# Kernel optimization log

Hardware: AMD Instinct MI355X
Metric: run time of the kernel (lower is better)

## Reference

```python
import jax, jax.numpy as jnp
import numpy as np

K_NN = 5
COS_EPS = 1e-8  # torch cosine_similarity eps


def setup_inputs() -> dict:
    key = jax.random.key(0)
    ks = jax.random.split(key, 10)
    N1, N2, D, E, H = 2000, 2000, 63, 64, 8
    return {
        "lm_X": jax.random.normal(ks[0], (N1, D), jnp.float32),
        "lm_Y": jax.random.normal(ks[1], (N1, 2), jnp.float32),
        "tg_X": jax.random.normal(ks[2], (N2, D), jnp.float32),
        "tg_Y": jax.random.normal(ks[3], (N2, 2), jnp.float32),
        "lm_delay": jax.random.uniform(ks[4], (N1,), jnp.float32),
        "tg_delay": jax.random.uniform(ks[5], (N2,), jnp.float32),
        # learned params: embedding Linear(input_dim=D+1 -> E) and per-head score weights
        "W_emb": jax.random.normal(ks[6], (E, D + 1), jnp.float32) / np.sqrt(D + 1),
        "b_emb": jnp.zeros((E,), jnp.float32),
        "w1": jax.random.normal(ks[7], (E, H), jnp.float32),
        "w2": jax.random.normal(ks[8], (E, H), jnp.float32),
    }


def _knn_adj(X, k):
    # binary row-wise k-nearest-neighbour adjacency, self excluded
    n = X.shape[0]
    sq = jnp.sum(X * X, axis=1)
    d2 = sq[:, None] + sq[None, :] - 2.0 * (X @ X.T)  # [n, n] squared distances
    d2 = jnp.where(jnp.eye(n, dtype=bool), jnp.inf, d2)  # exclude self
    _, idx = jax.lax.top_k(-d2, k)  # k smallest distances -> [n, k]
    rows = jnp.arange(n)[:, None]
    return jnp.zeros((n, n), X.dtype).at[rows, idx].set(1.0)


def reference(lm_X, lm_Y, tg_X, tg_Y, lm_delay, tg_delay, W_emb, b_emb, w1, w2):
    N1 = lm_X.shape[0]
    N2 = tg_X.shape[0]
    N = N1 + N2
    k = K_NN

    # ---- community-KNN adjacency over landmarks, label aggregation ----
    adj_lm = _knn_adj(lm_X, k)                      # [N1, N1] binary, k ones per row
    y_pred = (adj_lm @ lm_Y) * (1.0 / k)            # [N1, 2]

    # ---- teacher adjacency: (1 - I) with lm block = adj_lm, tg block = 0 ----
    adj_teacher = 1.0 - jnp.eye(N, dtype=lm_X.dtype)
    adj_teacher = adj_teacher.at[:N1, :N1].set(adj_lm)
    adj_teacher = adj_teacher.at[N1:, N1:].set(0.0)

    # ---- node features + embedding ----
    lm_feat = jnp.concatenate([lm_X, lm_delay[:, None]], axis=1)  # [N1, D+1]
    tg_feat = jnp.concatenate([tg_X, tg_delay[:, None]], axis=1)  # [N2, D+1]
    feats = jnp.concatenate([lm_feat, tg_feat], axis=0)           # [N, D+1]
    e = feats @ W_emb.T + b_emb                                    # [N, E]

    # ---- multi-head cosine-similarity edge probabilities (all heads at once) ----
    a = e[:, None, :] * w1.T[None, :, :]            # [N, H, E] : e * w1[:, h]
    b = e[:, None, :] * w2.T[None, :, :]            # [N, H, E] : e * w2[:, h]
    na = jnp.linalg.norm(a, axis=-1)                # [N, H]
    nb = jnp.linalg.norm(b, axis=-1)                # [N, H]
    dot = jnp.einsum("nhe,mhe->nmh", a, b)          # [N, N, H]
    sim = dot / jnp.maximum(na[:, None, :] * nb[None, :, :], COS_EPS)
    alpha = jax.nn.sigmoid(sim)                      # [N, N, H]
    adj = jnp.mean(alpha, axis=-1)                   # [N, N]

    return (y_pred, adj, adj_teacher)
```

## Files before the change

kernel.cpp:

```cpp
#include <hip/hip_runtime.h>
#include <math.h>

#define N1 2000
#define N2 2000
#define NT 4000
#define D  63
#define E  64
#define H  8
#define KNN 5
#define NPAD 4032
#define MPAD 4096

typedef short bf16x8 __attribute__((ext_vector_type(8)));
typedef float f32x4  __attribute__((ext_vector_type(4)));

__device__ __forceinline__ unsigned short f2bf(float x) {
    unsigned u = __float_as_uint(x);
    u = (u + 0x7fffu + ((u >> 16) & 1u)) >> 16;
    return (unsigned short)u;
}

__global__ void k_sq(const float* __restrict__ X, float* __restrict__ sq) {
    int i = blockIdx.x * blockDim.x + threadIdx.x;
    if (i < N1) {
        float s = 0.f;
        for (int d = 0; d < D; ++d) { float v = X[i * D + d]; s += v * v; }
        sq[i] = s;
    }
}

__global__ __launch_bounds__(256) void k_d2(const float* __restrict__ X,
                                            const float* __restrict__ sq,
                                            float* __restrict__ d2) {
    __shared__ float Xi[64][68];
    __shared__ float Xj[64][68];
    int i0 = blockIdx.y * 64, j0 = blockIdx.x * 64;
    int tid = threadIdx.x;
    for (int t = tid; t < 64 * 64; t += 256) {
        int r = t >> 6, c = t & 63;
        int gi = min(i0 + r, N1 - 1);
        int gj = min(j0 + r, N1 - 1);
        Xi[r][c] = (c < D) ? X[gi * D + c] : 0.f;
        Xj[r][c] = (c < D) ? X[gj * D + c] : 0.f;
    }
    __syncthreads();
    int tx = tid & 15, ty = tid >> 4;
    float acc[4][4];
    #pragma unroll
    for (int a = 0; a < 4; ++a)
        #pragma unroll
        for (int b = 0; b < 4; ++b) acc[a][b] = 0.f;

    #pragma unroll 4
    for (int kk = 0; kk < 16; ++kk) {
        float4 av[4], bv[4];
        #pragma unroll
        for (int ii = 0; ii < 4; ++ii) av[ii] = *(const float4*)&Xi[ty + 16 * ii][4 * kk];
        #pragma unroll
        for (int jj = 0; jj < 4; ++jj) bv[jj] = *(const float4*)&Xj[tx + 16 * jj][4 * kk];
        #pragma unroll
        for (int ii = 0; ii < 4; ++ii)
            #pragma unroll
            for (int jj = 0; jj < 4; ++jj)
                acc[ii][jj] += av[ii].x * bv[jj].x + av[ii].y * bv[jj].y +
                               av[ii].z * bv[jj].z + av[ii].w * bv[jj].w;
    }

    #pragma unroll
    for (int ii = 0; ii < 4; ++ii) {
        int i = i0 + ty + 16 * ii;
        #pragma unroll
        for (int jj = 0; jj < 4; ++jj) {
            int j = j0 + tx + 16 * jj;
            if (i < N1 && j < N1) {
                float v = sq[i] + sq[j] - 2.f * acc[ii][jj];
                if (i == j) v = __builtin_inff();
                d2[i * N1 + j] = v;
            }
        }
    }
}

__device__ __forceinline__ bool dless(float d1, int i1, float d2v, int i2) {
    return d1 < d2v || (d1 == d2v && i1 < i2);
}

__device__ __forceinline__ void ins5(float bd[KNN], int bi[KNN], float d, int j) {
    if (dless(d, j, bd[KNN - 1], bi[KNN - 1])) {
        bd[KNN - 1] = d; bi[KNN - 1] = j;
        #pragma unroll
        for (int s = KNN - 1; s > 0; --s) {
            if (dless(bd[s], bi[s], bd[s - 1], bi[s - 1])) {
                float td = bd[s]; bd[s] = bd[s - 1]; bd[s - 1] = td;
                int ti = bi[s]; bi[s] = bi[s - 1]; bi[s - 1] = ti;
            }
        }
    }
}

__global__ __launch_bounds__(256) void k_top5(const float* __restrict__ d2,
                                              const float* __restrict__ lmY,
                                              float* __restrict__ ypred,
                                              int* __restrict__ idx) {
    __shared__ float sd[4 * KNN];
    __shared__ int   si[4 * KNN];
    int i = blockIdx.x;
    int tid = threadIdx.x;
    const float* row = d2 + i * N1;

    float bd[KNN]; int bi[KNN];
    #pragma unroll
    for (int s = 0; s < KNN; ++s) { bd[s] = __builtin_inff(); bi[s] = 0x7fffffff; }
    #pragma unroll
    for (int k = 0; k < 8; ++k) {
        int j = tid + k * 256;
        if (j < N1) ins5(bd, bi, row[j], j);
    }

    int lane = tid & 63, wave = tid >> 6;
    float wd[KNN]; int wi[KNN];
    #pragma unroll
    for (int s = 0; s < KNN; ++s) {
        float d = bd[0]; int ix = bi[0];
        #pragma unroll
        for (int m = 1; m < 64; m <<= 1) {
            float od = __shfl_xor(d, m, 64);
            int   oi = __shfl_xor(ix, m, 64);
            if (dless(od, oi, d, ix)) { d = od; ix = oi; }
        }
        wd[s] = d; wi[s] = ix;
        if (d == bd[0] && ix == bi[0]) {
            #pragma unroll
            for (int q = 0; q < KNN - 1; ++q) { bd[q] = bd[q + 1]; bi[q] = bi[q + 1]; }
            bd[KNN - 1] = __builtin_inff(); bi[KNN - 1] = 0x7fffffff;
        }
    }
    if (lane == 0) {
        #pragma unroll
        for (int s = 0; s < KNN; ++s) { sd[wave * KNN + s] = wd[s]; si[wave * KNN + s] = wi[s]; }
    }
    __syncthreads();
    if (wave == 0) {
        float d = (lane < 4 * KNN) ? sd[lane] : __builtin_inff();
        int  ix = (lane < 4 * KNN) ? si[lane] : 0x7fffffff;
        float rd[KNN]; int ri[KNN];
        #pragma unroll
        for (int s = 0; s < KNN; ++s) {
            float md = d; int mi = ix;
            #pragma unroll
            for (int m = 1; m < 64; m <<= 1) {
                float od = __shfl_xor(md, m, 64);
                int   oi = __shfl_xor(mi, m, 64);
                if (dless(od, oi, md, mi)) { md = od; mi = oi; }
            }
            rd[s] = md; ri[s] = mi;
            if (md == d && mi == ix) { d = __builtin_inff(); ix = 0x7fffffff; }
        }
        if (lane == 0) {
            float y0 = 0.f, y1 = 0.f;
            #pragma unroll
            for (int s = 0; s < KNN; ++s) {
                int j = ri[s];
                y0 += lmY[j * 2];
                y1 += lmY[j * 2 + 1];
                idx[i * KNN + s] = j;
            }
            ypred[i * 2]     = y0 * 0.2f;
            ypred[i * 2 + 1] = y1 * 0.2f;
        }
    }
}

__global__ __launch_bounds__(256) void k_prep(const float* __restrict__ lmX,
                                              const float* __restrict__ tgX,
                                              const float* __restrict__ lmD,
                                              const float* __restrict__ tgD,
                                              const float* __restrict__ W,
                                              const float* __restrict__ bias,
                                              const float* __restrict__ w1,
                                              const float* __restrict__ w2,
                                              unsigned short* __restrict__ AL,
                                              unsigned short* __restrict__ Bbuf,
                                              float* __restrict__ sB) {
    __shared__ float f[4][E];
    __shared__ float Wl[E][68];
    int tid = threadIdx.x, lane = tid & 63, wave = tid >> 6;
    int n = blockIdx.x * 4 + wave;
    #pragma unroll
    for (int k = 0; k < 4; ++k) {
        int g = k * 256 + tid;
        float4 v = ((const float4*)W)[g];
        int r = g >> 4, c = (g & 15) * 4;
        *(float4*)&Wl[r][c] = v;
    }
    int t = lane;
    if (t < D)  f[wave][t] = (n < N1) ? lmX[n * D + t] : tgX[(n - N1) * D + t];
    if (t == D) f[wave][t] = (n < N1) ? lmD[n] : tgD[n - N1];
    __syncthreads();
    float s0 = 0.f, s1 = 0.f, s2 = 0.f, s3 = 0.f;
    #pragma unroll
    for (int k = 0; k < 16; ++k) {
        float4 wv = *(const float4*)&Wl[t][4 * k];
        float4 fv = *(const float4*)&f[wave][4 * k];
        s0 += fv.x * wv.x; s1 += fv.y * wv.y; s2 += fv.z * wv.z; s3 += fv.w * wv.w;
    }
    const float en = bias[t] + (s0 + s1) + (s2 + s3);
    Bbuf[n * E + t] = f2bf(en);

    int kc = t >> 5, kq = (t >> 3) & 3, j = t & 7;
    int alane = kq * 16 + (n & 15);
    int nb = n >> 4;
    #pragma unroll
    for (int h = 0; h < H; ++h) {
        float a = en * w1[t * H + h];
        float b = en * w2[t * H + h];
        float na2 = a * a, nb2 = b * b;
        #pragma unroll
        for (int m = 32; m >= 1; m >>= 1) {
            na2 += __shfl_xor(na2, m, 64);
            nb2 += __shfl_xor(nb2, m, 64);
        }
        float val = a * w2[t * H + h] * rsqrtf(na2);
        AL[(((nb * 8 + h) << 1) + kc) * 512 + alane * 8 + j] = f2bf(val);
        if (t == h) sB[n * H + h] = rsqrtf(nb2);
    }
}

__global__ __launch_bounds__(256) void k_adjm(const unsigned short* __restrict__ AL,
                                              const unsigned short* __restrict__ Bbuf,
                                              const float* __restrict__ sB,
                                              const int* __restrict__ idx,
                                              float* __restrict__ adj,
                                              float* __restrict__ adjT) {
    __shared__ unsigned short Bt[256][68];
    int tid = threadIdx.x;
    int m0 = blockIdx.x * 256, n0 = blockIdx.y * 64;

    #pragma unroll
    for (int it = 0; it < 8; ++it) {
        int g = it * 256 + tid;
        int row = g >> 3, c = g & 7;
        *(bf16x8*)&Bt[row][c * 8] = *(const bf16x8*)&Bbuf[(m0 + row) * E + c * 8];
    }

    int wave = tid >> 6, lane = tid & 63;
    int l15 = lane & 15, kq = lane >> 4;
    int nb = blockIdx.y * 4 + wave;

    bf16x8 afr[H][2];
    #pragma unroll
    for (int h = 0; h < H; ++h)
        #pragma unroll
        for (int kc = 0; kc < 2; ++kc)
            afr[h][kc] = *(const bf16x8*)&AL[(((nb * 8 + h) << 1) + kc) * 512 + lane * 8];

    __syncthreads();

    int nebase = n0 + wave * 16 + kq * 4;

    #pragma unroll 2
    for (int mt = 0; mt < 16; ++mt) {
        int mrow = mt * 16 + l15;
        int mcol = m0 + mrow;
        bf16x8 b0 = *(const bf16x8*)&Bt[mrow][kq * 8];
        bf16x8 b1 = *(const bf16x8*)&Bt[mrow][32 + kq * 8];

        float sbv[H];
        *(f32x4*)&sbv[0] = *(const f32x4*)&sB[mcol * H + 0];
        *(f32x4*)&sbv[4] = *(const f32x4*)&sB[mcol * H + 4];

        f32x4 acc[H];
        #pragma unroll
        for (int h = 0; h < H; ++h) {
            acc[h] = (f32x4){0.f, 0.f, 0.f, 0.f};
            acc[h] = __builtin_amdgcn_mfma_f32_16x16x32_bf16(afr[h][0], b0, acc[h], 0, 0, 0);
            acc[h] = __builtin_amdgcn_mfma_f32_16x16x32_bf16(afr[h][1], b1, acc[h], 0, 0, 0);
        }

        bool mok = (mcol < NT);
        #pragma unroll
        for (int reg = 0; reg < 4; ++reg) {
            int ne = nebase + reg;
            float sum = 0.f;
            #pragma unroll
            for (int h = 0; h < H; ++h) {
                float x = acc[h][reg] * sbv[h];
                float u = x * x;
                float p = fmaf(u, 1.8919e-3f, -2.0833333e-2f);
                p = fmaf(u, p, 0.25f);
                sum = fmaf(x, p, sum);
            }
            if (mok && ne < NT) adj[ne * NT + mcol] = fmaf(sum, 0.125f, 0.5f);
        }
    }

    #pragma unroll
    for (int it = 0; it < 16; ++it) {
        int g = it * 256 + tid;
        int r = g >> 6;
        int col = m0 + (g & 63) * 4;
        int row = n0 + r;
        if (row < NT && col < NT) {
            float v = ((row < N1) != (col < N1)) ? 1.f : 0.f;
            float4 o = {v, v, v, v};
            *(float4*)&adjT[row * NT + col] = o;
        }
    }
    __syncthreads();
    for (int p = tid; p < 64 * KNN; p += 256) {
        int r = p / KNN, s = p - r * KNN;
        int row = n0 + r;
        if (row < N1) {
            int jx = idx[row * KNN + s];
            if (jx >= m0 && jx < m0 + 256) adjT[row * NT + jx] = 1.f;
        }
    }
}

extern "C" void kernel_launch(void* const* d_in, const int* in_sizes, int n_in,
                              void* d_out, int out_size, void* d_ws, size_t ws_size,
                              hipStream_t stream) {
    const float* lmX  = (const float*)d_in[0];
    const float* lmY  = (const float*)d_in[1];
    const float* tgX  = (const float*)d_in[2];
    const float* lmD  = (const float*)d_in[4];
    const float* tgD  = (const float*)d_in[5];
    const float* Wemb = (const float*)d_in[6];
    const float* bemb = (const float*)d_in[7];
    const float* w1   = (const float*)d_in[8];
    const float* w2   = (const float*)d_in[9];

    float* out   = (float*)d_out;
    float* ypred = out;
    float* adj   = out + 4000;
    float* adjT  = out + 4000 + 16000000;

    char* ws = (char*)d_ws;
    unsigned short* AL   = (unsigned short*)ws;
    unsigned short* Bbuf = (unsigned short*)(ws + 4128768);
    float*          sB   = (float*)(ws + 4128768 + 524288);
    float*          sq   = (float*)(ws + 4784128);
    int*            idx  = (int*)  (ws + 4792128);

    float* d2 = adj;

    k_sq<<<(N1 + 255) / 256, 256, 0, stream>>>(lmX, sq);
    dim3 g2((N1 + 63) / 64, (N1 + 63) / 64);
    k_d2<<<g2, 256, 0, stream>>>(lmX, sq, d2);
    k_top5<<<N1, 256, 0, stream>>>(d2, lmY, ypred, idx);
    k_prep<<<NT / 4, 256, 0, stream>>>(lmX, tgX, lmD, tgD, Wemb, bemb, w1, w2,
                                       AL, Bbuf, sB);
    dim3 ga(MPAD / 256, NPAD / 64);
    k_adjm<<<ga, 256, 0, stream>>>(AL, Bbuf, sB, idx, adj, adjT);
}
```

Measured before the change: 224.7 us.

## Fuse distance computation with per-tile top-5 selection and interleave teacher writes

```diff
diff --git a/kernel.cpp b/kernel.cpp
--- a/kernel.cpp
+++ b/kernel.cpp
@@ -10,6 +10,7 @@
 #define KNN 5
 #define NPAD 4032
 #define MPAD 4096
+#define NCB 8
 
 typedef short bf16x8 __attribute__((ext_vector_type(8)));
 typedef float f32x4  __attribute__((ext_vector_type(4)));
@@ -20,67 +21,6 @@
     return (unsigned short)u;
 }
 
-__global__ void k_sq(const float* __restrict__ X, float* __restrict__ sq) {
-    int i = blockIdx.x * blockDim.x + threadIdx.x;
-    if (i < N1) {
-        float s = 0.f;
-        for (int d = 0; d < D; ++d) { float v = X[i * D + d]; s += v * v; }
-        sq[i] = s;
-    }
-}
-
-__global__ __launch_bounds__(256) void k_d2(const float* __restrict__ X,
-                                            const float* __restrict__ sq,
-                                            float* __restrict__ d2) {
-    __shared__ float Xi[64][68];
-    __shared__ float Xj[64][68];
-    int i0 = blockIdx.y * 64, j0 = blockIdx.x * 64;
-    int tid = threadIdx.x;
-    for (int t = tid; t < 64 * 64; t += 256) {
-        int r = t >> 6, c = t & 63;
-        int gi = min(i0 + r, N1 - 1);
-        int gj = min(j0 + r, N1 - 1);
-        Xi[r][c] = (c < D) ? X[gi * D + c] : 0.f;
-        Xj[r][c] = (c < D) ? X[gj * D + c] : 0.f;
-    }
-    __syncthreads();
-    int tx = tid & 15, ty = tid >> 4;
-    float acc[4][4];
-    #pragma unroll
-    for (int a = 0; a < 4; ++a)
-        #pragma unroll
-        for (int b = 0; b < 4; ++b) acc[a][b] = 0.f;
-
-    #pragma unroll 4
-    for (int kk = 0; kk < 16; ++kk) {
-        float4 av[4], bv[4];
-        #pragma unroll
-        for (int ii = 0; ii < 4; ++ii) av[ii] = *(const float4*)&Xi[ty + 16 * ii][4 * kk];
-        #pragma unroll
-        for (int jj = 0; jj < 4; ++jj) bv[jj] = *(const float4*)&Xj[tx + 16 * jj][4 * kk];
-        #pragma unroll
-        for (int ii = 0; ii < 4; ++ii)
-            #pragma unroll
-            for (int jj = 0; jj < 4; ++jj)
-                acc[ii][jj] += av[ii].x * bv[jj].x + av[ii].y * bv[jj].y +
-                               av[ii].z * bv[jj].z + av[ii].w * bv[jj].w;
-    }
-
-    #pragma unroll
-    for (int ii = 0; ii < 4; ++ii) {
-        int i = i0 + ty + 16 * ii;
-        #pragma unroll
-        for (int jj = 0; jj < 4; ++jj) {
-            int j = j0 + tx + 16 * jj;
-            if (i < N1 && j < N1) {
-                float v = sq[i] + sq[j] - 2.f * acc[ii][jj];
-                if (i == j) v = __builtin_inff();
-                d2[i * N1 + j] = v;
-            }
-        }
-    }
-}
-
 __device__ __forceinline__ bool dless(float d1, int i1, float d2v, int i2) {
     return d1 < d2v || (d1 == d2v && i1 < i2);
 }
@@ -98,76 +38,165 @@
     }
 }
 
-__global__ __launch_bounds__(256) void k_top5(const float* __restrict__ d2,
-                                              const float* __restrict__ lmY,
-                                              float* __restrict__ ypred,
-                                              int* __restrict__ idx) {
-    __shared__ float sd[4 * KNN];
-    __shared__ int   si[4 * KNN];
-    int i = blockIdx.x;
+__global__ __launch_bounds__(256) void k_knn(const float* __restrict__ X,
+                                             float* __restrict__ part_d,
+                                             int* __restrict__ part_i) {
+    __shared__ float Xi[64][68];
+    __shared__ float Xj[64][68];
+    __shared__ float sqi[64];
+    __shared__ float sqj[64];
+    int cb = blockIdx.x, rb = blockIdx.y;
+    int i0 = rb * 64;
     int tid = threadIdx.x;
-    const float* row = d2 + i * N1;
-
-    float bd[KNN]; int bi[KNN];
-    #pragma unroll
-    for (int s = 0; s < KNN; ++s) { bd[s] = __builtin_inff(); bi[s] = 0x7fffffff; }
-    #pragma unroll
-    for (int k = 0; k < 8; ++k) {
-        int j = tid + k * 256;
-        if (j < N1) ins5(bd, bi, row[j], j);
-    }
-
-    int lane = tid & 63, wave = tid >> 6;
-    float wd[KNN]; int wi[KNN];
+
+    for (int t = tid; t < 64 * 64; t += 256) {
+        int r = t >> 6, c = t & 63;
+        int gi = min(i0 + r, N1 - 1);
+        Xi[r][c] = (c < D) ? X[gi * D + c] : 0.f;
+    }
+    __syncthreads();
+    if (tid < 64) {
+        float s = 0.f;
+        #pragma unroll
+        for (int q = 0; q < 16; ++q) {
+            float4 v = *(const float4*)&Xi[tid][4 * q];
+            s += v.x * v.x + v.y * v.y + v.z * v.z + v.w * v.w;
+        }
+        sqi[tid] = s;
+    }
+
+    int tx = tid & 15, ty = tid >> 4;
+    float bd[4][KNN]; int bi[4][KNN];
+    #pragma unroll
+    for (int ii = 0; ii < 4; ++ii)
+        #pragma unroll
+        for (int s = 0; s < KNN; ++s) { bd[ii][s] = __builtin_inff(); bi[ii][s] = 0x7fffffff; }
+
+    for (int js = 0; js < 4; ++js) {
+        int j0 = cb * 256 + js * 64;
+        if (j0 >= N1) break;
+        __syncthreads();
+        for (int t = tid; t < 64 * 64; t += 256) {
+            int r = t >> 6, c = t & 63;
+            int gj = min(j0 + r, N1 - 1);
+            Xj[r][c] = (c < D) ? X[gj * D + c] : 0.f;
+        }
+        __syncthreads();
+        if (tid < 64) {
+            float s = 0.f;
+            #pragma unroll
+            for (int q = 0; q < 16; ++q) {
+                float4 v = *(const float4*)&Xj[tid][4 * q];
+                s += v.x * v.x + v.y * v.y + v.z * v.z + v.w * v.w;
+            }
+            sqj[tid] = s;
+        }
+        __syncthreads();
+
+        float acc[4][4];
+        #pragma unroll
+        for (int a = 0; a < 4; ++a)
+            #pragma unroll
+            for (int b = 0; b < 4; ++b) acc[a][b] = 0.f;
+
+        #pragma unroll 4
+        for (int kk = 0; kk < 16; ++kk) {
+            float4 av[4], bv[4];
+            #pragma unroll
+            for (int ii = 0; ii < 4; ++ii) av[ii] = *(const float4*)&Xi[ty + 16 * ii][4 * kk];
+            #pragma unroll
+            for (int jj = 0; jj < 4; ++jj) bv[jj] = *(const float4*)&Xj[tx + 16 * jj][4 * kk];
+            #pragma unroll
+            for (int ii = 0; ii < 4; ++ii)
+                #pragma unroll
+                for (int jj = 0; jj < 4; ++jj)
+                    acc[ii][jj] += av[ii].x * bv[jj].x + av[ii].y * bv[jj].y +
+                                   av[ii].z * bv[jj].z + av[ii].w * bv[jj].w;
+        }
+
+        #pragma unroll
+        for (int ii = 0; ii < 4; ++ii) {
+            int gi = i0 + ty + 16 * ii;
+            float si = sqi[ty + 16 * ii];
+            #pragma unroll
+            for (int jj = 0; jj < 4; ++jj) {
+                int gj = j0 + tx + 16 * jj;
+                if (gj < N1 && gj != gi) {
+                    float dv = si + sqj[tx + 16 * jj] - 2.f * acc[ii][jj];
+                    ins5(bd[ii], bi[ii], dv, gj);
+                }
+            }
+        }
+    }
+
+    #pragma unroll
+    for (int ii = 0; ii < 4; ++ii) {
+        float wd[KNN]; int wi[KNN];
+        #pragma unroll
+        for (int s = 0; s < KNN; ++s) {
+            float d = bd[ii][0]; int ix = bi[ii][0];
+            #pragma unroll
+            for (int m = 1; m < 16; m <<= 1) {
+                float od = __shfl_xor(d, m, 64);
+                int   oi = __shfl_xor(ix, m, 64);
+                if (dless(od, oi, d, ix)) { d = od; ix = oi; }
+            }
+            wd[s] = d; wi[s] = ix;
+            if (d == bd[ii][0] && ix == bi[ii][0]) {
+                #pragma unroll
+                for (int q = 0; q < KNN - 1; ++q) { bd[ii][q] = bd[ii][q + 1]; bi[ii][q] = bi[ii][q + 1]; }
+                bd[ii][KNN - 1] = __builtin_inff(); bi[ii][KNN - 1] = 0x7fffffff;
+            }
+        }
+        if (tx == 0) {
+            int row = i0 + ty + 16 * ii;
+            if (row < N1) {
+                #pragma unroll
+                for (int s = 0; s < KNN; ++s) {
+                    part_d[row * (NCB * KNN) + cb * KNN + s] = wd[s];
+                    part_i[row * (NCB * KNN) + cb * KNN + s] = wi[s];
+                }
+            }
+        }
+    }
+}
+
+__global__ __launch_bounds__(256) void k_merge(const float* __restrict__ part_d,
+                                               const int* __restrict__ part_i,
+                                               const float* __restrict__ lmY,
+                                               float* __restrict__ ypred,
+                                               int* __restrict__ idx) {
+    int wave = threadIdx.x >> 6, lane = threadIdx.x & 63;
+    int row = blockIdx.x * 4 + wave;
+    float d = __builtin_inff(); int ix = 0x7fffffff;
+    if (lane < NCB * KNN) {
+        d  = part_d[row * (NCB * KNN) + lane];
+        ix = part_i[row * (NCB * KNN) + lane];
+    }
+    float rd[KNN]; int ri[KNN];
     #pragma unroll
     for (int s = 0; s < KNN; ++s) {
-        float d = bd[0]; int ix = bi[0];
+        float md = d; int mi = ix;
         #pragma unroll
         for (int m = 1; m < 64; m <<= 1) {
-            float od = __shfl_xor(d, m, 64);
-            int   oi = __shfl_xor(ix, m, 64);
-            if (dless(od, oi, d, ix)) { d = od; ix = oi; }
-        }
-        wd[s] = d; wi[s] = ix;
-        if (d == bd[0] && ix == bi[0]) {
-            #pragma unroll
-            for (int q = 0; q < KNN - 1; ++q) { bd[q] = bd[q + 1]; bi[q] = bi[q + 1]; }
-            bd[KNN - 1] = __builtin_inff(); bi[KNN - 1] = 0x7fffffff;
-        }
+            float od = __shfl_xor(md, m, 64);
+            int   oi = __shfl_xor(mi, m, 64);
+            if (dless(od, oi, md, mi)) { md = od; mi = oi; }
+        }
+        rd[s] = md; ri[s] = mi;
+        if (md == d && mi == ix) { d = __builtin_inff(); ix = 0x7fffffff; }
     }
     if (lane == 0) {
-        #pragma unroll
-        for (int s = 0; s < KNN; ++s) { sd[wave * KNN + s] = wd[s]; si[wave * KNN + s] = wi[s]; }
-    }
-    __syncthreads();
-    if (wave == 0) {
-        float d = (lane < 4 * KNN) ? sd[lane] : __builtin_inff();
-        int  ix = (lane < 4 * KNN) ? si[lane] : 0x7fffffff;
-        float rd[KNN]; int ri[KNN];
+        float y0 = 0.f, y1 = 0.f;
         #pragma unroll
         for (int s = 0; s < KNN; ++s) {
-            float md = d; int mi = ix;
-            #pragma unroll
-            for (int m = 1; m < 64; m <<= 1) {
-                float od = __shfl_xor(md, m, 64);
-                int   oi = __shfl_xor(mi, m, 64);
-                if (dless(od, oi, md, mi)) { md = od; mi = oi; }
-            }
-            rd[s] = md; ri[s] = mi;
-            if (md == d && mi == ix) { d = __builtin_inff(); ix = 0x7fffffff; }
-        }
-        if (lane == 0) {
-            float y0 = 0.f, y1 = 0.f;
-            #pragma unroll
-            for (int s = 0; s < KNN; ++s) {
-                int j = ri[s];
-                y0 += lmY[j * 2];
-                y1 += lmY[j * 2 + 1];
-                idx[i * KNN + s] = j;
-            }
-            ypred[i * 2]     = y0 * 0.2f;
-            ypred[i * 2 + 1] = y1 * 0.2f;
-        }
+            int j = ri[s];
+            y0 += lmY[j * 2];
+            y1 += lmY[j * 2 + 1];
+            idx[row * KNN + s] = j;
+        }
+        ypred[row * 2]     = y0 * 0.2f;
+        ypred[row * 2 + 1] = y1 * 0.2f;
     }
 }
 
@@ -257,9 +286,19 @@
     __syncthreads();
 
     int nebase = n0 + wave * 16 + kq * 4;
+    int tr = tid >> 2, tcq = tid & 3;
 
     #pragma unroll 2
     for (int mt = 0; mt < 16; ++mt) {
+        {
+            int row = n0 + tr, col = m0 + mt * 16 + tcq * 4;
+            if (row < NT && col < NT) {
+                float v = ((row < N1) != (col < N1)) ? 1.f : 0.f;
+                float4 o = {v, v, v, v};
+                *(float4*)&adjT[row * NT + col] = o;
+            }
+        }
+
         int mrow = mt * 16 + l15;
         int mcol = m0 + mrow;
         bf16x8 b0 = *(const bf16x8*)&Bt[mrow][kq * 8];
@@ -294,18 +333,6 @@
         }
     }
 
-    #pragma unroll
-    for (int it = 0; it < 16; ++it) {
-        int g = it * 256 + tid;
-        int r = g >> 6;
-        int col = m0 + (g & 63) * 4;
-        int row = n0 + r;
-        if (row < NT && col < NT) {
-            float v = ((row < N1) != (col < N1)) ? 1.f : 0.f;
-            float4 o = {v, v, v, v};
-            *(float4*)&adjT[row * NT + col] = o;
-        }
-    }
     __syncthreads();
     for (int p = tid; p < 64 * KNN; p += 256) {
         int r = p / KNN, s = p - r * KNN;
@@ -336,18 +363,16 @@
     float* adjT  = out + 4000 + 16000000;
 
     char* ws = (char*)d_ws;
-    unsigned short* AL   = (unsigned short*)ws;
-    unsigned short* Bbuf = (unsigned short*)(ws + 4128768);
-    float*          sB   = (float*)(ws + 4128768 + 524288);
-    float*          sq   = (float*)(ws + 4784128);
-    int*            idx  = (int*)  (ws + 4792128);
-
-    float* d2 = adj;
-
-    k_sq<<<(N1 + 255) / 256, 256, 0, stream>>>(lmX, sq);
-    dim3 g2((N1 + 63) / 64, (N1 + 63) / 64);
-    k_d2<<<g2, 256, 0, stream>>>(lmX, sq, d2);
-    k_top5<<<N1, 256, 0, stream>>>(d2, lmY, ypred, idx);
+    unsigned short* AL    = (unsigned short*)ws;
+    unsigned short* Bbuf  = (unsigned short*)(ws + 4128768);
+    float*          sB    = (float*)(ws + 4128768 + 524288);
+    float*          partd = (float*)(ws + 4784128);
+    int*            parti = (int*)  (ws + 5104128);
+    int*            idx   = (int*)  (ws + 5424128);
+
+    dim3 gk(NCB, 32);
+    k_knn<<<gk, 256, 0, stream>>>(lmX, partd, parti);
+    k_merge<<<N1 / 4, 256, 0, stream>>>(partd, parti, lmY, ypred, idx);
     k_prep<<<NT / 4, 256, 0, stream>>>(lmX, tgX, lmD, tgD, Wemb, bemb, w1, w2,
                                        AL, Bbuf, sB);
     dim3 ga(MPAD / 256, NPAD / 64);
```

New measurement: 239.4 us. +6.5%, slower.
